# Performance work log

Hardware: AMD Instinct MI355X
Metric: run time of the kernel (lower is better)

Reference implementation:

```python
import jax, jax.numpy as jnp
import numpy as np

B, S, HN, TN = 8, 32, 64, 512
HID, EMB, VOCAB = 512, 512, 10000


def setup_inputs():
    key = jax.random.key(0)
    k = jax.random.split(key, 14)
    w = lambda kk, shape: jax.random.normal(kk, shape, jnp.float32) * 0.02
    return {
        "dec_out": jax.random.normal(k[0], (B, S, HID), jnp.float32),
        "history": jax.random.normal(k[1], (B, HID), jnp.float32),
        "head": jax.random.randint(k[2], (B, HN), 0, VOCAB),
        "tail": jax.random.randint(k[3], (B, TN), 0, VOCAB),
        "adj_mask": jax.random.randint(k[4], (B, HN, TN), 0, 2).astype(bool),
        "dup_mask": jax.random.randint(k[5], (B, S, TN), 0, 2).astype(bool),
        "emb_table": w(k[6], (VOCAB, EMB)),
        "W_tq": w(k[7], (2 * HID + EMB, HID)),
        "b_tq": jnp.zeros((HID,), jnp.float32),
        "W_tk": w(k[8], (EMB, HID)),
        "b_tk": jnp.zeros((HID,), jnp.float32),
        "W_tout": w(k[9], (2 * HID, HID)),
        "W_hq": w(k[10], (2 * HID, HID)),
        "b_hq": jnp.zeros((HID,), jnp.float32),
        "W_hk": w(k[11], (HID, HID)),
        "b_hk": jnp.zeros((HID,), jnp.float32),
    }


def reference(dec_out, history, head, tail, adj_mask, dup_mask, emb_table,
              W_tq, b_tq, W_tk, b_tk, W_tout, W_hq, b_hq, W_hk, b_hk):
    head_emb = emb_table[head]  # (B, HN, EMB)
    tail_emb = emb_table[tail]  # (B, TN, EMB)

    # --- tail attention query: Linear(cat([dec_out, history, head_emb])) + ELU.
    # Same math as the torch broadcast-concat, computed as a sum of three
    # partial matmuls to avoid materializing the (B,S,HN,2*hid+emb) concat.
    Wd, Wh, We = W_tq[:HID], W_tq[HID:2 * HID], W_tq[2 * HID:]
    tq = jax.nn.elu((dec_out @ Wd)[:, :, None, :]
                    + (history @ Wh)[:, None, None, :]
                    + (head_emb @ We)[:, None, :, :]
                    + b_tq)                       # (B, S, HN, HID)
    tq = tq.reshape(B, S * HN, HID)
    tk = jax.nn.elu(tail_emb @ W_tk + b_tk)       # (B, TN, HID)  (dropout=eval)

    # combined logical mask: allowed = adjacency AND not-duplicate
    mask = (adj_mask[:, None, :, :] & ~dup_mask[:, :, None, :]).reshape(B, S * HN, TN)

    # GlobalAttention (dot): score -> mask -> softmax -> context -> tanh(linear_out([c;q]))
    scores = jnp.einsum('bqh,bth->bqt', tq, tk)   # (B, S*HN, TN)
    tail_attn = jax.nn.softmax(jnp.where(mask, scores, -jnp.inf), axis=-1)
    ctx = jnp.einsum('bqt,bth->bqh', tail_attn, tk)
    graph_hid = jnp.tanh(ctx @ W_tout[:HID] + tq @ W_tout[HID:])
    graph_hid = graph_hid.reshape(B * S, HN, HID)
    tail_attn = tail_attn.reshape(B * S, HN, TN)

    # --- head attention (one-step), length-masked over HN
    hq = jax.nn.elu(dec_out @ W_hq[:HID] + (history @ W_hq[HID:])[:, None, :] + b_hq)
    hq = hq.reshape(B * S, HID)
    hk = jax.nn.elu(jnp.einsum('nkh,hd->nkd', graph_hid, W_hk) + b_hk)
    lengths = jnp.repeat(jnp.sum(head != 0, axis=-1), S)          # (B*S,)
    hscores = jnp.einsum('nh,nkh->nk', hq, hk)                    # (B*S, HN)
    lmask = jnp.arange(HN)[None, :] < lengths[:, None]
    head_attn = jax.nn.softmax(jnp.where(lmask, hscores, -jnp.inf), axis=-1)
    # (head-attention context output is discarded by the original module)

    prob = jnp.einsum('nk,nkt->nt', head_attn, tail_attn).reshape(B, S, TN)
    return jnp.log(prob + 1e-20)
```

## Files before the change

### kernel.cpp

```cpp
#include <hip/hip_runtime.h>
#include <math.h>

#define BB 8
#define SS 32
#define HN 64
#define TN 512
#define HID 512

typedef __attribute__((ext_vector_type(8))) short short8;
typedef __attribute__((ext_vector_type(4))) float f32x4;

__device__ __forceinline__ float eluf(float x) { return x > 0.f ? x : (expf(x) - 1.f); }

__device__ __forceinline__ short f2bs(float f) {
    union { float f; unsigned int u; } v; v.f = f;
    unsigned int r = v.u + 0x7fffu + ((v.u >> 16) & 1u);
    return (short)(r >> 16);
}
__device__ __forceinline__ float b2f(short s) {
    union { unsigned int u; float f; } v;
    v.u = ((unsigned int)(unsigned short)s) << 16;
    return v.f;
}

__device__ __forceinline__ void gld16(const void* g, void* l) {
    __builtin_amdgcn_global_load_lds(
        (const __attribute__((address_space(1))) void*)g,
        (__attribute__((address_space(3))) void*)l, 16, 0, 0);
}

template <int ACT, int OUTB>
__device__ __forceinline__ void gcore(
    const short* __restrict__ A, const short* __restrict__ B,
    const float* __restrict__ bias, void* __restrict__ Cv,
    int ldc, int K, int m0, int n0, int cm0, short* Ls)
{
    short* Al = Ls;
    short* Bl = Ls + 8192;
    const int tid  = threadIdx.x;
    const int lane = tid & 63;
    const int w    = tid >> 6;
    const int wr   = w >> 1, wc = w & 1;
    const int l16  = lane & 15, quad = lane >> 4;

    const int srow = w * 16 + (lane >> 2);
    const int scol = (lane & 3) * 8;

    f32x4 acc[4][4];
#pragma unroll
    for (int i = 0; i < 4; ++i)
#pragma unroll
        for (int j = 0; j < 4; ++j) { acc[i][j][0]=0.f; acc[i][j][1]=0.f; acc[i][j][2]=0.f; acc[i][j][3]=0.f; }

    short* lA = Al + w * 512;
    short* lB = Bl + w * 512;
    const long rstep = (long)64 * K;

    const short* Ag = A + (long)(m0 + srow) * K + scol;
    const short* Bg = B + (long)(n0 + srow) * K + scol;
    for (int kt = 0; kt < K; kt += 64) {
        __syncthreads();
        gld16(Ag + kt, lA);
        gld16(Ag + kt + rstep, lA + 2048);
        gld16(Ag + kt + 32, lA + 4096);
        gld16(Ag + kt + 32 + rstep, lA + 4096 + 2048);
        gld16(Bg + kt, lB);
        gld16(Bg + kt + rstep, lB + 2048);
        gld16(Bg + kt + 32, lB + 4096);
        gld16(Bg + kt + 32 + rstep, lB + 4096 + 2048);
        __syncthreads();
#pragma unroll
        for (int h = 0; h < 2; ++h) {
            short8 af[4], bf4[4];
#pragma unroll
            for (int mi = 0; mi < 4; ++mi)
                af[mi] = *(const short8*)(Al + h * 4096 + (wr * 64 + mi * 16 + l16) * 32 + quad * 8);
#pragma unroll
            for (int ni = 0; ni < 4; ++ni)
                bf4[ni] = *(const short8*)(Bl + h * 4096 + (wc * 64 + ni * 16 + l16) * 32 + quad * 8);
#pragma unroll
            for (int mi = 0; mi < 4; ++mi)
#pragma unroll
                for (int ni = 0; ni < 4; ++ni)
                    acc[mi][ni] = __builtin_amdgcn_mfma_f32_16x16x32_bf16(af[mi], bf4[ni], acc[mi][ni], 0, 0, 0);
        }
    }

    __syncthreads();

    float bv[4];
#pragma unroll
    for (int ni = 0; ni < 4; ++ni)
        bv[ni] = bias ? bias[n0 + wc * 64 + ni * 16 + l16] : 0.f;

    if (OUTB == 1) {
        short* eb = Ls + w * 1152;
        const int er = lane >> 2;
        const int ec = (lane & 3) * 16;
#pragma unroll
        for (int mi = 0; mi < 4; ++mi) {
#pragma unroll
            for (int ni = 0; ni < 4; ++ni)
#pragma unroll
                for (int r = 0; r < 4; ++r) {
                    float x = acc[mi][ni][r] + bv[ni];
                    if (ACT == 1) x = eluf(x);
                    eb[(quad * 4 + r) * 72 + ni * 16 + l16] = f2bs(x);
                }
            __builtin_amdgcn_sched_barrier(0);
            short8 v0 = *(const short8*)&eb[er * 72 + ec];
            short8 v1 = *(const short8*)&eb[er * 72 + ec + 8];
            long cb = (long)(cm0 + wr * 64 + mi * 16 + er) * ldc + n0 + wc * 64 + ec;
            *(short8*)((short*)Cv + cb)     = v0;
            *(short8*)((short*)Cv + cb + 8) = v1;
            __builtin_amdgcn_sched_barrier(0);
        }
    } else {
#pragma unroll
        for (int mi = 0; mi < 4; ++mi)
#pragma unroll
            for (int ni = 0; ni < 4; ++ni) {
                int gc = n0 + wc * 64 + ni * 16 + l16;
#pragma unroll
                for (int r = 0; r < 4; ++r) {
                    float x = acc[mi][ni][r] + bv[ni];
                    if (ACT == 1) x = eluf(x);
                    ((float*)Cv)[(long)(cm0 + wr * 64 + mi * 16 + quad * 4 + r) * ldc + gc] = x;
                }
            }
    }
}

#define L_TQ   0
#define L_BST  32768
#define L_AST  65536
#define L_EB   69632
#define L_HQ   78848
#define L_TOT  79872

template <int AFT>
__device__ __forceinline__ void tgemmv(
    const short* __restrict__ Arows, const short* __restrict__ B,
    short* Ls, f32x4 (&acc)[4][4])
{
    const int tid  = threadIdx.x;
    const int lane = tid & 63;
    const int w    = tid >> 6;
    const int l16  = lane & 15, quad = lane >> 4;
    short* TQ  = Ls + L_TQ;
    short* BST = Ls + L_BST;
    short* AST = Ls + L_AST;

    auto STAGE = [&](int kt, int p) {
        short* Bl = BST + p * 16384;
#pragma unroll
        for (int j = 0; j < 4; ++j) {
            int lin = j * 512 + tid;
            int r = lin >> 2, gs = lin & 3;
            int g = gs ^ ((r >> 1) & 3);
            gld16(B + (long)r * 512 + kt + g * 8, Bl + j * 4096 + w * 512);
        }
        if constexpr (AFT == 0) {
            if (tid < 256) {
                short* Al = AST + p * 2048;
                int r = tid >> 2, gs = tid & 3;
                int g = gs ^ ((r >> 1) & 3);
                gld16(Arows + (long)r * 512 + kt + g * 8, Al + w * 512);
            }
        }
    };

    STAGE(0, 0);
    int p = 0;
    for (int kt = 0; kt < 512; kt += 32, p ^= 1) {
        if (kt + 32 < 512) {
            STAGE(kt + 32, p ^ 1);
            if (AFT == 0 && w < 4) asm volatile("s_waitcnt vmcnt(5)" ::: "memory");
            else                   asm volatile("s_waitcnt vmcnt(4)" ::: "memory");
        } else {
            asm volatile("s_waitcnt vmcnt(0)" ::: "memory");
        }
        __builtin_amdgcn_s_barrier();
        __builtin_amdgcn_sched_barrier(0);

        short* Bl = BST + p * 16384;
        short8 af[4], bf[4];
#pragma unroll
        for (int mi = 0; mi < 4; ++mi) {
            int row = mi * 16 + l16;
            if constexpr (AFT == 1) {
                int slot = ((kt >> 3) + quad) ^ (row & 7);
                af[mi] = *(const short8*)(TQ + row * 512 + slot * 8);
            } else {
                short* Al = AST + p * 2048;
                int slot = quad ^ ((row >> 1) & 3);
                af[mi] = *(const short8*)(Al + row * 32 + slot * 8);
            }
        }
#pragma unroll
        for (int ni = 0; ni < 4; ++ni) {
            int row = w * 64 + ni * 16 + l16;
            int slot = quad ^ ((row >> 1) & 3);
            bf[ni] = *(const short8*)(Bl + row * 32 + slot * 8);
        }
#pragma unroll
        for (int mi = 0; mi < 4; ++mi)
#pragma unroll
            for (int ni = 0; ni < 4; ++ni)
                acc[mi][ni] = __builtin_amdgcn_mfma_f32_16x16x32_bf16(af[mi], bf[ni], acc[mi][ni], 0, 0, 0);
        asm volatile("s_waitcnt lgkmcnt(0)" ::: "memory");
        __builtin_amdgcn_s_barrier();
        __builtin_amdgcn_sched_barrier(0);
    }
}

template <int MODE>
__device__ __forceinline__ void epi(f32x4 (&acc)[4][4], short* Ls)
{
    const int tid  = threadIdx.x;
    const int lane = tid & 63;
    const int w    = tid >> 6;
    const int l16  = lane & 15, quad = lane >> 4;
    short* eb = Ls + L_EB + w * 1152;
    const int er = lane >> 2;
    const int ec = (lane & 3) * 16;
#pragma unroll
    for (int mi = 0; mi < 4; ++mi) {
#pragma unroll
        for (int ni = 0; ni < 4; ++ni)
#pragma unroll
            for (int r = 0; r < 4; ++r) {
                float x = acc[mi][ni][r];
                if (MODE == 1) x = tanhf(x);
                eb[(quad * 4 + r) * 72 + ni * 16 + l16] = f2bs(x);
            }
        __builtin_amdgcn_sched_barrier(0);
        short8 v0 = *(const short8*)&eb[er * 72 + ec];
        short8 v1 = *(const short8*)&eb[er * 72 + ec + 8];
        int row = mi * 16 + er;
        if (MODE == 0) {
            short* SC = Ls + L_BST;
            *(short8*)(SC + row * 512 + w * 64 + ec)     = v0;
            *(short8*)(SC + row * 512 + w * 64 + ec + 8) = v1;
        } else {
            int g0 = (w * 64 + ec) >> 3;
            *(short8*)(Ls + L_TQ + row * 512 + ((g0)     ^ (row & 7)) * 8) = v0;
            *(short8*)(Ls + L_TQ + row * 512 + ((g0 + 1) ^ (row & 7)) * 8) = v1;
        }
        __builtin_amdgcn_sched_barrier(0);
    }
}

__global__ __launch_bounds__(512, 1) void tail_kernel(
    const float* __restrict__ qall, const float* __restrict__ qe,
    const float* __restrict__ b_tq, const float* __restrict__ b_hq,
    const short* __restrict__ tkb, const short* __restrict__ tkWTb,
    const short* __restrict__ WT,
    const int* __restrict__ adj, const int* __restrict__ dup,
    const int* __restrict__ head, const float* __restrict__ b_hk,
    short* __restrict__ Pb, float* __restrict__ out)
{
    __shared__ short Ls[L_TOT];
    const int tid  = threadIdx.x;
    const int lane = tid & 63;
    const int w    = tid >> 6;
    const int l16  = lane & 15, quad = lane >> 4;

    const int n = (blockIdx.x & 7) * 32 + (blockIdx.x >> 3);
    const int b = n >> 5;
    const int s = n & 31;
    const long rb = (long)n * 64;

    const short* tkb_b  = tkb + (long)b * 262144;
    const short* tkWT_b = tkWTb + (long)b * 262144;
    const short* WT7    = WT + (size_t)7 * 262144;
    const short* WT8    = WT + (size_t)8 * 262144;
    short* Prows = Pb + rb * 512;
    float* HQ = (float*)(Ls + L_HQ);

    {
        const int cg = tid & 63;
        const int wg = tid >> 6;
        float4 qd0 = *(const float4*)(qall + (long)n * 2048 + cg * 8);
        float4 qd1 = *(const float4*)(qall + (long)n * 2048 + cg * 8 + 4);
        float4 qh0 = *(const float4*)(qall + (long)(256 + b) * 2048 + 1024 + cg * 8);
        float4 qh1 = *(const float4*)(qall + (long)(256 + b) * 2048 + 1024 + cg * 8 + 4);
        float4 bt0 = *(const float4*)(b_tq + cg * 8);
        float4 bt1 = *(const float4*)(b_tq + cg * 8 + 4);
        float base[8] = {qd0.x + qh0.x + bt0.x, qd0.y + qh0.y + bt0.y,
                         qd0.z + qh0.z + bt0.z, qd0.w + qh0.w + bt0.w,
                         qd1.x + qh1.x + bt1.x, qd1.y + qh1.y + bt1.y,
                         qd1.z + qh1.z + bt1.z, qd1.w + qh1.w + bt1.w};
#pragma unroll
        for (int i = 0; i < 8; ++i) {
            int h = wg * 8 + i;
            const float* er = qe + (long)(b * 64 + h) * 512 + cg * 8;
            float4 e0 = *(const float4*)er;
            float4 e1 = *(const float4*)(er + 4);
            float ev[8] = {e0.x, e0.y, e0.z, e0.w, e1.x, e1.y, e1.z, e1.w};
            short8 o;
#pragma unroll
            for (int u = 0; u < 8; ++u) o[u] = f2bs(eluf(base[u] + ev[u]));
            int slot = cg ^ (h & 7);
            *(short8*)(Ls + L_TQ + h * 512 + slot * 8) = o;
        }
        if (tid < 512) {
            HQ[tid] = eluf(qall[(long)n * 2048 + 512 + tid]
                         + qall[(long)(256 + b) * 2048 + 1536 + tid] + b_hq[tid]);
        }
    }
    __syncthreads();

    f32x4 acc[4][4];
#pragma unroll
    for (int i = 0; i < 4; ++i)
#pragma unroll
        for (int j = 0; j < 4; ++j) { acc[i][j][0]=0.f; acc[i][j][1]=0.f; acc[i][j][2]=0.f; acc[i][j][3]=0.f; }

    tgemmv<1>(nullptr, tkb_b, Ls, acc);
    epi<0>(acc, Ls);
    __syncthreads();

    {
        short* SC = Ls + L_BST;
        const int* dupr = dup + ((long)(b * 32 + s)) * 512 + lane * 8;
        int4 d0 = *(const int4*)dupr, d1 = *(const int4*)(dupr + 4);
        int dm[8] = {d0.x, d0.y, d0.z, d0.w, d1.x, d1.y, d1.z, d1.w};
        for (int j = 0; j < 8; ++j) {
            int row = w * 8 + j;
            short8 v8 = *(const short8*)(SC + row * 512 + lane * 8);
            const int* adjr = adj + ((long)(b * 64 + row)) * 512 + lane * 8;
            int4 a0 = *(const int4*)adjr, a1 = *(const int4*)(adjr + 4);
            int am[8] = {a0.x, a0.y, a0.z, a0.w, a1.x, a1.y, a1.z, a1.w};
            float v[8];
            float m = -INFINITY;
#pragma unroll
            for (int i = 0; i < 8; ++i) {
                v[i] = (am[i] && !dm[i]) ? b2f(v8[i]) : -INFINITY;
                m = fmaxf(m, v[i]);
            }
#pragma unroll
            for (int d = 32; d >= 1; d >>= 1) m = fmaxf(m, __shfl_xor(m, d));
            float sum = 0.f;
#pragma unroll
            for (int i = 0; i < 8; ++i) {
                float e = (m == -INFINITY) ? 0.f : expf(v[i] - m);
                v[i] = e; sum += e;
            }
#pragma unroll
            for (int d = 32; d >= 1; d >>= 1) sum += __shfl_xor(sum, d);
            float inv = sum > 0.f ? 1.f / sum : 0.f;
            short8 o;
#pragma unroll
            for (int i = 0; i < 8; ++i) o[i] = f2bs(v[i] * inv);
            *(short8*)(Prows + (long)row * 512 + lane * 8) = o;
        }
    }
    __syncthreads();

#pragma unroll
    for (int i = 0; i < 4; ++i)
#pragma unroll
        for (int j = 0; j < 4; ++j) { acc[i][j][0]=0.f; acc[i][j][1]=0.f; acc[i][j][2]=0.f; acc[i][j][3]=0.f; }
    tgemmv<1>(nullptr, WT7, Ls, acc);
    tgemmv<0>(Prows, tkWT_b, Ls, acc);
    epi<1>(acc, Ls);
    __syncthreads();

#pragma unroll
    for (int i = 0; i < 4; ++i)
#pragma unroll
        for (int j = 0; j < 4; ++j) { acc[i][j][0]=0.f; acc[i][j][1]=0.f; acc[i][j][2]=0.f; acc[i][j][3]=0.f; }
    tgemmv<1>(nullptr, WT8, Ls, acc);

    float* F     = (float*)(Ls + L_BST);
    float* redf  = F;
    float* hal   = F + 512;
    float* partf = F + 576;
    {
        float bv[4], hqv[4];
#pragma unroll
        for (int ni = 0; ni < 4; ++ni) {
            int col = w * 64 + ni * 16 + l16;
            bv[ni]  = b_hk[col];
            hqv[ni] = HQ[col];
        }
#pragma unroll
        for (int mi = 0; mi < 4; ++mi)
#pragma unroll
            for (int r = 0; r < 4; ++r) {
                float p = 0.f;
#pragma unroll
                for (int ni = 0; ni < 4; ++ni)
                    p += eluf(acc[mi][ni][r] + bv[ni]) * hqv[ni];
                p += __shfl_xor(p, 1);
                p += __shfl_xor(p, 2);
                p += __shfl_xor(p, 4);
                p += __shfl_xor(p, 8);
                if (l16 == 0) redf[w * 64 + mi * 16 + quad * 4 + r] = p;
            }
    }
    __syncthreads();

    if (tid < 64) {
        float sv_raw = 0.f;
#pragma unroll
        for (int w2 = 0; w2 < 8; ++w2) sv_raw += redf[w2 * 64 + tid];
        int hv = head[b * 64 + tid];
        unsigned long long ball = __ballot(hv != 0);
        int len = __popcll(ball);
        float sv = (tid < len) ? sv_raw : -INFINITY;
        float m = sv;
#pragma unroll
        for (int d = 32; d >= 1; d >>= 1) m = fmaxf(m, __shfl_xor(m, d));
        float e = expf(sv - m);
        float sum = e;
#pragma unroll
        for (int d = 32; d >= 1; d >>= 1) sum += __shfl_xor(sum, d);
        hal[tid] = e / sum;
    }
    __syncthreads();

    {
        const short* tab = Prows + (long)(w * 8) * 512 + lane * 8;
        float a2[8] = {};
#pragma unroll
        for (int k = 0; k < 8; ++k) {
            float a = hal[w * 8 + k];
            short8 tv = *(const short8*)(tab + (long)k * 512);
#pragma unroll
            for (int u = 0; u < 8; ++u) a2[u] += a * b2f(tv[u]);
        }
        float4* pp = (float4*)&partf[w * 512 + lane * 8];
        pp[0] = make_float4(a2[0], a2[1], a2[2], a2[3]);
        pp[1] = make_float4(a2[4], a2[5], a2[6], a2[7]);
    }
    __syncthreads();

    {
        float a = 0.f;
#pragma unroll
        for (int w2 = 0; w2 < 8; ++w2) a += partf[w2 * 512 + tid];
        out[(long)n * 512 + tid] = logf(a + 1e-20f);
    }
}

struct WTDesc { const float* src[9]; short* dst[9]; };

__global__ __launch_bounds__(256) void prep(
    const float* __restrict__ dec_out, const float* __restrict__ history,
    short* __restrict__ decb,
    const float* __restrict__ emb, const int* __restrict__ head, const int* __restrict__ tail,
    short* __restrict__ embAll, WTDesc wd)
{
    __shared__ float t[32][33];
    const int id = blockIdx.x, tid = threadIdx.x;
    if (id < 132) {
        int i = (id * 256 + tid) * 4;
        float4 v = (i < 131072) ? *(const float4*)(dec_out + i)
                                : *(const float4*)(history + (i - 131072));
        short4 o;
        o.x = f2bs(v.x); o.y = f2bs(v.y); o.z = f2bs(v.z); o.w = f2bs(v.w);
        *(short4*)(decb + i) = o;
    } else if (id < 132 + 2304) {
        int r = (id - 132) * 2 + (tid >> 7);
        int c4 = (tid & 127) * 4;
        int idx = (r < 512) ? head[r] : tail[r - 512];
        float4 v = *(const float4*)(emb + (long)idx * 512 + c4);
        short4 o;
        o.x = f2bs(v.x); o.y = f2bs(v.y); o.z = f2bs(v.z); o.w = f2bs(v.w);
        *(short4*)(embAll + (long)r * 512 + c4) = o;
    } else {
        int q = id - 2436;
        int z = q >> 8, xy = q & 255;
        int x = xy & 15, y = xy >> 4;
        const float* src = wd.src[z];
        short* dst = wd.dst[z];
        int k0 = y * 32, n0 = x * 32;
        int tx = tid & 31, ty = tid >> 5;
#pragma unroll
        for (int i = 0; i < 32; i += 8)
            t[ty + i][tx] = src[(long)(k0 + ty + i) * 512 + n0 + tx];
        __syncthreads();
#pragma unroll
        for (int i = 0; i < 32; i += 8)
            dst[(long)(n0 + ty + i) * 512 + k0 + tx] = f2bs(t[tx][ty + i]);
    }
}

__global__ __launch_bounds__(256) void mgemm_multi(
    const short* __restrict__ decb, const short* __restrict__ WTall, float* __restrict__ qall,
    const short* __restrict__ embAll, const short* __restrict__ WTe, float* __restrict__ qe,
    const short* __restrict__ WTk, const float* __restrict__ b_tk, short* __restrict__ tkb)
{
    __shared__ short Ls[16384];
    int id = blockIdx.x;
    if (id < 48) {
        int y = id >> 4, x = id & 15;
        gcore<0, 0>(decb, WTall, nullptr, qall, 2048, 512, y * 128, x * 128, y * 128, Ls);
    } else if (id < 64) {
        int id2 = id - 48, y = id2 >> 2, x = id2 & 3;
        gcore<0, 0>(embAll, WTe, nullptr, qe, 512, 512, y * 128, x * 128, y * 128, Ls);
    } else {
        int id3 = id - 64, y = id3 >> 2, x = id3 & 3;
        gcore<1, 1>(embAll, WTk, b_tk, tkb, 512, 512, 512 + y * 128, x * 128, y * 128, Ls);
    }
}

__global__ __launch_bounds__(256) void tkwt_kernel(
    const short* __restrict__ WTo1, const short* __restrict__ tkb, short* __restrict__ tkWTb)
{
    __shared__ short Ls[16384];
    int id = blockIdx.x;
    int z = id >> 4, r = id & 15;
    int x = r & 3, y = r >> 2;
    gcore<0, 1>(WTo1, tkb + (long)z * 262144, nullptr,
                tkWTb + (long)z * 262144, 512, 512, y * 128, x * 128, y * 128, Ls);
}

extern "C" void kernel_launch(void* const* d_in, const int* in_sizes, int n_in,
                              void* d_out, int out_size, void* d_ws, size_t ws_size,
                              hipStream_t stream)
{
    const float* dec_out = (const float*)d_in[0];
    const float* history = (const float*)d_in[1];
    const int*   head    = (const int*)d_in[2];
    const int*   tail    = (const int*)d_in[3];
    const int*   adj     = (const int*)d_in[4];
    const int*   dup     = (const int*)d_in[5];
    const float* emb     = (const float*)d_in[6];
    const float* W_tq    = (const float*)d_in[7];
    const float* b_tq    = (const float*)d_in[8];
    const float* W_tk    = (const float*)d_in[9];
    const float* b_tk    = (const float*)d_in[10];
    const float* W_tout  = (const float*)d_in[11];
    const float* W_hq    = (const float*)d_in[12];
    const float* b_hq    = (const float*)d_in[13];
    const float* W_hk    = (const float*)d_in[14];
    const float* b_hk    = (const float*)d_in[15];
    float* out = (float*)d_out;

    char* ws = (char*)d_ws;
    auto alloc = [&](size_t bytes) -> void* {
        char* p = ws;
        ws += (bytes + 255) & ~(size_t)255;
        return (void*)p;
    };
    short* decb   = (short*)alloc((size_t)384 * 512 * 2);
    short* embAll = (short*)alloc((size_t)4608 * 512 * 2);
    short* WT     = (short*)alloc((size_t)9 * 512 * 512 * 2);
    float* qall   = (float*)alloc((size_t)384 * 2048 * 4);
    float* qe     = (float*)alloc((size_t)512 * 512 * 4);
    short* tkb    = (short*)alloc((size_t)4096 * 512 * 2);
    short* tkWTb  = (short*)alloc((size_t)4096 * 512 * 2);
    short* Pb     = (short*)alloc((size_t)16384 * 512 * 2);

    WTDesc wd;
    wd.src[0] = W_tq;               wd.dst[0] = WT;
    wd.src[1] = W_hq;               wd.dst[1] = WT + (size_t)1 * 262144;
    wd.src[2] = W_tq + 512 * 512;   wd.dst[2] = WT + (size_t)2 * 262144;
    wd.src[3] = W_hq + 512 * 512;   wd.dst[3] = WT + (size_t)3 * 262144;
    wd.src[4] = W_tq + 1024 * 512;  wd.dst[4] = WT + (size_t)4 * 262144;
    wd.src[5] = W_tk;               wd.dst[5] = WT + (size_t)5 * 262144;
    wd.src[6] = W_tout;             wd.dst[6] = WT + (size_t)6 * 262144;
    wd.src[7] = W_tout + 512 * 512; wd.dst[7] = WT + (size_t)7 * 262144;
    wd.src[8] = W_hk;               wd.dst[8] = WT + (size_t)8 * 262144;

    prep<<<4740, 256, 0, stream>>>(dec_out, history, decb, emb, head, tail, embAll, wd);
    mgemm_multi<<<192, 256, 0, stream>>>(decb, WT, qall, embAll, WT + (size_t)4 * 262144, qe,
                                         WT + (size_t)5 * 262144, b_tk, tkb);
    tkwt_kernel<<<128, 256, 0, stream>>>(WT + (size_t)6 * 262144, tkb, tkWTb);
    tail_kernel<<<256, 512, 0, stream>>>(qall, qe, b_tq, b_hq, tkb, tkWTb, WT,
                                         adj, dup, head, b_hk, Pb, out);
}
```

Measured before the change: 198.8 us.

## Keep attention probabilities in LDS and read GEMM B operands directly from global

```diff
diff --git a/kernel.cpp b/kernel.cpp
--- a/kernel.cpp
+++ b/kernel.cpp
@@ -132,85 +132,38 @@
 }
 
 #define L_TQ   0
-#define L_BST  32768
-#define L_AST  65536
-#define L_EB   69632
-#define L_HQ   78848
-#define L_TOT  79872
-
-template <int AFT>
-__device__ __forceinline__ void tgemmv(
-    const short* __restrict__ Arows, const short* __restrict__ B,
-    short* Ls, f32x4 (&acc)[4][4])
+#define L_SC   32768
+#define L_EBF  65536
+#define L_HQ   75008
+#define L_TOT  76032
+
+__device__ __forceinline__ void tgemmd(
+    const short* As , const short* __restrict__ B,
+    f32x4 (&acc)[4][4])
 {
     const int tid  = threadIdx.x;
     const int lane = tid & 63;
     const int w    = tid >> 6;
     const int l16  = lane & 15, quad = lane >> 4;
-    short* TQ  = Ls + L_TQ;
-    short* BST = Ls + L_BST;
-    short* AST = Ls + L_AST;
-
-    auto STAGE = [&](int kt, int p) {
-        short* Bl = BST + p * 16384;
-#pragma unroll
-        for (int j = 0; j < 4; ++j) {
-            int lin = j * 512 + tid;
-            int r = lin >> 2, gs = lin & 3;
-            int g = gs ^ ((r >> 1) & 3);
-            gld16(B + (long)r * 512 + kt + g * 8, Bl + j * 4096 + w * 512);
-        }
-        if constexpr (AFT == 0) {
-            if (tid < 256) {
-                short* Al = AST + p * 2048;
-                int r = tid >> 2, gs = tid & 3;
-                int g = gs ^ ((r >> 1) & 3);
-                gld16(Arows + (long)r * 512 + kt + g * 8, Al + w * 512);
-            }
-        }
-    };
-
-    STAGE(0, 0);
-    int p = 0;
-    for (int kt = 0; kt < 512; kt += 32, p ^= 1) {
-        if (kt + 32 < 512) {
-            STAGE(kt + 32, p ^ 1);
-            if (AFT == 0 && w < 4) asm volatile("s_waitcnt vmcnt(5)" ::: "memory");
-            else                   asm volatile("s_waitcnt vmcnt(4)" ::: "memory");
-        } else {
-            asm volatile("s_waitcnt vmcnt(0)" ::: "memory");
-        }
-        __builtin_amdgcn_s_barrier();
-        __builtin_amdgcn_sched_barrier(0);
-
-        short* Bl = BST + p * 16384;
+    const short* Bw = B + (long)(w * 64 + l16) * 512 + quad * 8;
+
+#pragma unroll 2
+    for (int kt = 0; kt < 512; kt += 32) {
         short8 af[4], bf[4];
+#pragma unroll
+        for (int ni = 0; ni < 4; ++ni)
+            bf[ni] = *(const short8*)(Bw + (long)(ni * 16) * 512 + kt);
 #pragma unroll
         for (int mi = 0; mi < 4; ++mi) {
             int row = mi * 16 + l16;
-            if constexpr (AFT == 1) {
-                int slot = ((kt >> 3) + quad) ^ (row & 7);
-                af[mi] = *(const short8*)(TQ + row * 512 + slot * 8);
-            } else {
-                short* Al = AST + p * 2048;
-                int slot = quad ^ ((row >> 1) & 3);
-                af[mi] = *(const short8*)(Al + row * 32 + slot * 8);
-            }
-        }
-#pragma unroll
-        for (int ni = 0; ni < 4; ++ni) {
-            int row = w * 64 + ni * 16 + l16;
-            int slot = quad ^ ((row >> 1) & 3);
-            bf[ni] = *(const short8*)(Bl + row * 32 + slot * 8);
+            int slot = ((kt >> 3) + quad) ^ (row & 7);
+            af[mi] = *(const short8*)(As + row * 512 + slot * 8);
         }
 #pragma unroll
         for (int mi = 0; mi < 4; ++mi)
 #pragma unroll
             for (int ni = 0; ni < 4; ++ni)
                 acc[mi][ni] = __builtin_amdgcn_mfma_f32_16x16x32_bf16(af[mi], bf[ni], acc[mi][ni], 0, 0, 0);
-        asm volatile("s_waitcnt lgkmcnt(0)" ::: "memory");
-        __builtin_amdgcn_s_barrier();
-        __builtin_amdgcn_sched_barrier(0);
     }
 }
 
@@ -221,7 +174,7 @@
     const int lane = tid & 63;
     const int w    = tid >> 6;
     const int l16  = lane & 15, quad = lane >> 4;
-    short* eb = Ls + L_EB + w * 1152;
+    short* eb = Ls + L_EBF + w * 1152;
     const int er = lane >> 2;
     const int ec = (lane & 3) * 16;
 #pragma unroll
@@ -239,9 +192,8 @@
         short8 v1 = *(const short8*)&eb[er * 72 + ec + 8];
         int row = mi * 16 + er;
         if (MODE == 0) {
-            short* SC = Ls + L_BST;
-            *(short8*)(SC + row * 512 + w * 64 + ec)     = v0;
-            *(short8*)(SC + row * 512 + w * 64 + ec + 8) = v1;
+            *(short8*)(Ls + L_SC + row * 512 + w * 64 + ec)     = v0;
+            *(short8*)(Ls + L_SC + row * 512 + w * 64 + ec + 8) = v1;
         } else {
             int g0 = (w * 64 + ec) >> 3;
             *(short8*)(Ls + L_TQ + row * 512 + ((g0)     ^ (row & 7)) * 8) = v0;
@@ -249,6 +201,13 @@
         }
         __builtin_amdgcn_sched_barrier(0);
     }
+}
+
+__device__ __forceinline__ void zacc(f32x4 (&acc)[4][4]) {
+#pragma unroll
+    for (int i = 0; i < 4; ++i)
+#pragma unroll
+        for (int j = 0; j < 4; ++j) { acc[i][j][0]=0.f; acc[i][j][1]=0.f; acc[i][j][2]=0.f; acc[i][j][3]=0.f; }
 }
 
 __global__ __launch_bounds__(512, 1) void tail_kernel(
@@ -258,7 +217,7 @@
     const short* __restrict__ WT,
     const int* __restrict__ adj, const int* __restrict__ dup,
     const int* __restrict__ head, const float* __restrict__ b_hk,
-    short* __restrict__ Pb, float* __restrict__ out)
+    float* __restrict__ out)
 {
     __shared__ short Ls[L_TOT];
     const int tid  = threadIdx.x;
@@ -269,14 +228,13 @@
     const int n = (blockIdx.x & 7) * 32 + (blockIdx.x >> 3);
     const int b = n >> 5;
     const int s = n & 31;
-    const long rb = (long)n * 64;
 
     const short* tkb_b  = tkb + (long)b * 262144;
     const short* tkWT_b = tkWTb + (long)b * 262144;
     const short* WT7    = WT + (size_t)7 * 262144;
     const short* WT8    = WT + (size_t)8 * 262144;
-    short* Prows = Pb + rb * 512;
     float* HQ = (float*)(Ls + L_HQ);
+    short* SC = Ls + L_SC;
 
     {
         const int cg = tid & 63;
@@ -304,25 +262,19 @@
             int slot = cg ^ (h & 7);
             *(short8*)(Ls + L_TQ + h * 512 + slot * 8) = o;
         }
-        if (tid < 512) {
-            HQ[tid] = eluf(qall[(long)n * 2048 + 512 + tid]
-                         + qall[(long)(256 + b) * 2048 + 1536 + tid] + b_hq[tid]);
-        }
+        HQ[tid] = eluf(qall[(long)n * 2048 + 512 + tid]
+                     + qall[(long)(256 + b) * 2048 + 1536 + tid] + b_hq[tid]);
     }
     __syncthreads();
 
     f32x4 acc[4][4];
-#pragma unroll
-    for (int i = 0; i < 4; ++i)
-#pragma unroll
-        for (int j = 0; j < 4; ++j) { acc[i][j][0]=0.f; acc[i][j][1]=0.f; acc[i][j][2]=0.f; acc[i][j][3]=0.f; }
-
-    tgemmv<1>(nullptr, tkb_b, Ls, acc);
+    zacc(acc);
+
+    tgemmd(Ls + L_TQ, tkb_b, acc);
     epi<0>(acc, Ls);
     __syncthreads();
 
     {
-        short* SC = Ls + L_BST;
         const int* dupr = dup + ((long)(b * 32 + s)) * 512 + lane * 8;
         int4 d0 = *(const int4*)dupr, d1 = *(const int4*)(dupr + 4);
         int dm[8] = {d0.x, d0.y, d0.z, d0.w, d1.x, d1.y, d1.z, d1.w};
@@ -353,27 +305,22 @@
             short8 o;
 #pragma unroll
             for (int i = 0; i < 8; ++i) o[i] = f2bs(v[i] * inv);
-            *(short8*)(Prows + (long)row * 512 + lane * 8) = o;
-        }
-    }
-    __syncthreads();
-
-#pragma unroll
-    for (int i = 0; i < 4; ++i)
-#pragma unroll
-        for (int j = 0; j < 4; ++j) { acc[i][j][0]=0.f; acc[i][j][1]=0.f; acc[i][j][2]=0.f; acc[i][j][3]=0.f; }
-    tgemmv<1>(nullptr, WT7, Ls, acc);
-    tgemmv<0>(Prows, tkWT_b, Ls, acc);
+            *(short8*)(SC + row * 512 + (lane ^ (row & 7)) * 8) = o;
+        }
+    }
+    __syncthreads();
+
+    zacc(acc);
+    tgemmd(Ls + L_TQ, WT7, acc);
+    tgemmd(SC, tkWT_b, acc);
+    __syncthreads();
     epi<1>(acc, Ls);
     __syncthreads();
 
-#pragma unroll
-    for (int i = 0; i < 4; ++i)
-#pragma unroll
-        for (int j = 0; j < 4; ++j) { acc[i][j][0]=0.f; acc[i][j][1]=0.f; acc[i][j][2]=0.f; acc[i][j][3]=0.f; }
-    tgemmv<1>(nullptr, WT8, Ls, acc);
-
-    float* F     = (float*)(Ls + L_BST);
+    zacc(acc);
+    tgemmd(Ls + L_TQ, WT8, acc);
+
+    float* F     = (float*)(Ls + L_EBF);
     float* redf  = F;
     float* hal   = F + 512;
     float* partf = F + 576;
@@ -422,12 +369,12 @@
     __syncthreads();
 
     {
-        const short* tab = Prows + (long)(w * 8) * 512 + lane * 8;
         float a2[8] = {};
 #pragma unroll
         for (int k = 0; k < 8; ++k) {
-            float a = hal[w * 8 + k];
-            short8 tv = *(const short8*)(tab + (long)k * 512);
+            int row = w * 8 + k;
+            float a = hal[row];
+            short8 tv = *(const short8*)(SC + row * 512 + (lane ^ (row & 7)) * 8);
 #pragma unroll
             for (int u = 0; u < 8; ++u) a2[u] += a * b2f(tv[u]);
         }
@@ -553,7 +500,6 @@
     float* qe     = (float*)alloc((size_t)512 * 512 * 4);
     short* tkb    = (short*)alloc((size_t)4096 * 512 * 2);
     short* tkWTb  = (short*)alloc((size_t)4096 * 512 * 2);
-    short* Pb     = (short*)alloc((size_t)16384 * 512 * 2);
 
     WTDesc wd;
     wd.src[0] = W_tq;               wd.dst[0] = WT;
@@ -571,5 +517,5 @@
                                          WT + (size_t)5 * 262144, b_tk, tkb);
     tkwt_kernel<<<128, 256, 0, stream>>>(WT + (size_t)6 * 262144, tkb, tkWTb);
     tail_kernel<<<256, 512, 0, stream>>>(qall, qe, b_tq, b_hq, tkb, tkWTb, WT,
-                                         adj, dup, head, b_hk, Pb, out);
-}
+                                         adj, dup, head, b_hk, out);
+}
```

After: 215.9 us. 8.6% more time.

## Use per-wave private B staging to drop block barriers in TQ GEMMs

Applied to the files above, without the earlier changes.

```diff
diff --git a/kernel.cpp b/kernel.cpp
--- a/kernel.cpp
+++ b/kernel.cpp
@@ -138,16 +138,62 @@
 #define L_HQ   78848
 #define L_TOT  79872
 
-template <int AFT>
-__device__ __forceinline__ void tgemmv(
-    const short* __restrict__ Arows, const short* __restrict__ B,
-    short* Ls, f32x4 (&acc)[4][4])
+__device__ __forceinline__ void tgemmw(
+    const short* TQ, const short* __restrict__ B, short* Ls, f32x4 (&acc)[4][4])
 {
     const int tid  = threadIdx.x;
     const int lane = tid & 63;
     const int w    = tid >> 6;
     const int l16  = lane & 15, quad = lane >> 4;
-    short* TQ  = Ls + L_TQ;
+    short* BW = Ls + L_BST + w * 2048;
+
+    auto STAGE = [&](int kt, int p) {
+        short* dst = BW + p * 16384;
+#pragma unroll
+        for (int j = 0; j < 4; ++j)
+            gld16(B + (long)(w * 64 + j * 16 + (lane >> 2)) * 512 + kt + (lane & 3) * 8,
+                  dst + j * 512);
+    };
+
+    STAGE(0, 0);
+    int p = 0;
+    for (int kt = 0; kt < 512; kt += 32, p ^= 1) {
+        asm volatile("s_waitcnt lgkmcnt(0)" ::: "memory");
+        if (kt + 32 < 512) {
+            STAGE(kt + 32, p ^ 1);
+            asm volatile("s_waitcnt vmcnt(4)" ::: "memory");
+        } else {
+            asm volatile("s_waitcnt vmcnt(0)" ::: "memory");
+        }
+        __builtin_amdgcn_sched_barrier(0);
+
+        short* Bl = BW + p * 16384;
+        short8 af[4], bf[4];
+#pragma unroll
+        for (int mi = 0; mi < 4; ++mi) {
+            int row = mi * 16 + l16;
+            int slot = ((kt >> 3) + quad) ^ (row & 7);
+            af[mi] = *(const short8*)(TQ + row * 512 + slot * 8);
+        }
+#pragma unroll
+        for (int ni = 0; ni < 4; ++ni)
+            bf[ni] = *(const short8*)(Bl + (ni * 16 + l16) * 32 + quad * 8);
+#pragma unroll
+        for (int mi = 0; mi < 4; ++mi)
+#pragma unroll
+            for (int ni = 0; ni < 4; ++ni)
+                acc[mi][ni] = __builtin_amdgcn_mfma_f32_16x16x32_bf16(af[mi], bf[ni], acc[mi][ni], 0, 0, 0);
+    }
+}
+
+__device__ __forceinline__ void tgemmp(
+    const short* __restrict__ Arows, const short* __restrict__ B,
+    short* Ls, f32x4 (&acc)[4][4])
+{
+    const int tid  = threadIdx.x;
+    const int lane = tid & 63;
+    const int w    = tid >> 6;
+    const int l16  = lane & 15, quad = lane >> 4;
     short* BST = Ls + L_BST;
     short* AST = Ls + L_AST;
 
@@ -160,13 +206,11 @@
             int g = gs ^ ((r >> 1) & 3);
             gld16(B + (long)r * 512 + kt + g * 8, Bl + j * 4096 + w * 512);
         }
-        if constexpr (AFT == 0) {
-            if (tid < 256) {
-                short* Al = AST + p * 2048;
-                int r = tid >> 2, gs = tid & 3;
-                int g = gs ^ ((r >> 1) & 3);
-                gld16(Arows + (long)r * 512 + kt + g * 8, Al + w * 512);
-            }
+        if (tid < 256) {
+            short* Al = AST + p * 2048;
+            int r = tid >> 2, gs = tid & 3;
+            int g = gs ^ ((r >> 1) & 3);
+            gld16(Arows + (long)r * 512 + kt + g * 8, Al + w * 512);
         }
     };
 
@@ -175,8 +219,8 @@
     for (int kt = 0; kt < 512; kt += 32, p ^= 1) {
         if (kt + 32 < 512) {
             STAGE(kt + 32, p ^ 1);
-            if (AFT == 0 && w < 4) asm volatile("s_waitcnt vmcnt(5)" ::: "memory");
-            else                   asm volatile("s_waitcnt vmcnt(4)" ::: "memory");
+            if (w < 4) asm volatile("s_waitcnt vmcnt(5)" ::: "memory");
+            else       asm volatile("s_waitcnt vmcnt(4)" ::: "memory");
         } else {
             asm volatile("s_waitcnt vmcnt(0)" ::: "memory");
         }
@@ -184,18 +228,13 @@
         __builtin_amdgcn_sched_barrier(0);
 
         short* Bl = BST + p * 16384;
+        short* Al = AST + p * 2048;
         short8 af[4], bf[4];
 #pragma unroll
         for (int mi = 0; mi < 4; ++mi) {
             int row = mi * 16 + l16;
-            if constexpr (AFT == 1) {
-                int slot = ((kt >> 3) + quad) ^ (row & 7);
-                af[mi] = *(const short8*)(TQ + row * 512 + slot * 8);
-            } else {
-                short* Al = AST + p * 2048;
-                int slot = quad ^ ((row >> 1) & 3);
-                af[mi] = *(const short8*)(Al + row * 32 + slot * 8);
-            }
+            int slot = quad ^ ((row >> 1) & 3);
+            af[mi] = *(const short8*)(Al + row * 32 + slot * 8);
         }
 #pragma unroll
         for (int ni = 0; ni < 4; ++ni) {
@@ -317,7 +356,8 @@
 #pragma unroll
         for (int j = 0; j < 4; ++j) { acc[i][j][0]=0.f; acc[i][j][1]=0.f; acc[i][j][2]=0.f; acc[i][j][3]=0.f; }
 
-    tgemmv<1>(nullptr, tkb_b, Ls, acc);
+    tgemmw(Ls + L_TQ, tkb_b, Ls, acc);
+    __syncthreads();
     epi<0>(acc, Ls);
     __syncthreads();
 
@@ -362,8 +402,9 @@
     for (int i = 0; i < 4; ++i)
 #pragma unroll
         for (int j = 0; j < 4; ++j) { acc[i][j][0]=0.f; acc[i][j][1]=0.f; acc[i][j][2]=0.f; acc[i][j][3]=0.f; }
-    tgemmv<1>(nullptr, WT7, Ls, acc);
-    tgemmv<0>(Prows, tkWT_b, Ls, acc);
+    tgemmw(Ls + L_TQ, WT7, Ls, acc);
+    __syncthreads();
+    tgemmp(Prows, tkWT_b, Ls, acc);
     epi<1>(acc, Ls);
     __syncthreads();
 
@@ -371,7 +412,8 @@
     for (int i = 0; i < 4; ++i)
 #pragma unroll
         for (int j = 0; j < 4; ++j) { acc[i][j][0]=0.f; acc[i][j][1]=0.f; acc[i][j][2]=0.f; acc[i][j][3]=0.f; }
-    tgemmv<1>(nullptr, WT8, Ls, acc);
+    tgemmw(Ls + L_TQ, WT8, Ls, acc);
+    __syncthreads();
 
     float* F     = (float*)(Ls + L_BST);
     float* redf  = F;
```

After: 194.3 us. 2.3% less time.
